# Kernel optimization log

Hardware: AMD Instinct MI355X
Metric: run time of the kernel (lower is better)

## Reference

```python
import jax, jax.numpy as jnp
import numpy as np

N = 50000      # nodes
E = 600000     # edges
D = 128        # feature dim (ninput == noutput -> residual)
GN = 5000      # graph_node_size (10 graphs)
GE = 60000     # graph_edge_size
EPS_NORM = 1e-5
EPS_RED = 1e-6


def graph_norm(x, size, gamma, beta):
    # torch.split into equal graphs, per-graph mean / (std(ddof=1) + eps)
    G = x.shape[0] // size
    xr = x.reshape(G, size, -1)
    mean = xr.mean(axis=1, keepdims=True)
    std = jnp.std(xr, axis=1, keepdims=True, ddof=1)  # torch.std is unbiased
    out = ((xr - mean) / (std + EPS_NORM)).reshape(x.shape)
    return gamma * out + beta


def setup_inputs() -> dict:
    key = jax.random.key(0)
    ks = jax.random.split(key, 10)
    h = jax.random.normal(ks[0], (N, D), dtype=jnp.float32)
    e = jax.random.normal(ks[1], (E, D), dtype=jnp.float32)
    src = jax.random.randint(ks[2], (E,), 0, N, dtype=jnp.int32)
    dst = jax.random.randint(ks[3], (E,), 0, N, dtype=jnp.int32)
    snorm_n = jnp.ones((1,), jnp.float32)
    snorm_e = jnp.ones((1,), jnp.float32)
    # 5 Linear layers (fc1..fc5), stored as [in, out] so y = x @ W + b
    W = jax.random.normal(ks[4], (5, D, D), dtype=jnp.float32) * (1.0 / np.sqrt(D))
    b = jax.random.normal(ks[5], (5, D), dtype=jnp.float32) * 0.01
    gamma_h = jnp.ones((D,), jnp.float32)
    beta_h = jnp.zeros((D,), jnp.float32)
    gamma_e = jnp.ones((D,), jnp.float32)
    beta_e = jnp.zeros((D,), jnp.float32)
    return {"h": h, "e": e, "src": src, "dst": dst,
            "snorm_n": snorm_n, "snorm_e": snorm_e,
            "W": W, "b": b,
            "gamma_h": gamma_h, "beta_h": beta_h,
            "gamma_e": gamma_e, "beta_e": beta_e}


def reference(h, e, src, dst, snorm_n, snorm_e, W, b, gamma_h, beta_h, gamma_e, beta_e):
    h_in, e_in = h, e
    Ah = h @ W[0] + b[0]
    Bh = h @ W[1] + b[1]
    Ce = e @ W[2] + b[2]
    Dh = h @ W[3] + b[3]
    Eh = h @ W[4] + b[4]

    # message: e_ij = Ce + Dh[src] + Eh[dst]
    e_new = Ce + Dh[src] + Eh[dst]              # [E, D]
    sig = jax.nn.sigmoid(e_new)
    num = jax.ops.segment_sum(sig * Bh[src], dst, num_segments=N)   # [N, D]
    den = jax.ops.segment_sum(sig, dst, num_segments=N)             # [N, D]
    deg = jax.ops.segment_sum(jnp.ones((E, 1), h.dtype), dst, num_segments=N)
    h_agg = Ah + num / (den + EPS_RED)
    # DGL leaves zero-in-degree nodes untouched (keep original h)
    h_new = jnp.where(deg > 0, h_agg, h)

    h_new = h_new * snorm_n
    h_new = jax.nn.relu(graph_norm(h_new, GN, gamma_h, beta_h))
    e_out = e_new * snorm_e
    e_out = jax.nn.relu(graph_norm(e_out, GE, gamma_e, beta_e))

    # residual (ninput == noutput); dropout is identity in eval mode
    h_new = h_in + h_new
    e_out = e_in + e_out
    return (h_new, e_out)
```

## Files before the change

### kernel.cpp

```cpp
#include <hip/hip_runtime.h>
#include <math.h>

#define NNODES 50000
#define NEDGES 600000
#define DIM 128
#define GNSZ 5000
#define GESZ 60000
#define NDTOT (NNODES*DIM)
#define EPS_NORM 1e-5f
#define EPS_RED  1e-6f

union F4 { float4 v; float f[4]; };

__device__ __forceinline__ float4 ld4(const float* p){ return *(const float4*)p; }

__global__ __launch_bounds__(256) void k1_node_gemm(
    const float* __restrict__ h, const float* __restrict__ W, const float* __restrict__ bias,
    float* __restrict__ Ah, float* __restrict__ Bh, float* __restrict__ Dh, float* __restrict__ Eh)
{
  __shared__ float as[32][129];
  const int t = threadIdx.x;
  const int base = blockIdx.x * 32;
  #pragma unroll
  for (int i = 0; i < 4; i++){
    int f = t + i*256;
    int row = f >> 5, c4 = (f & 31) * 4;
    float4 v = make_float4(0.f,0.f,0.f,0.f);
    if (base + row < NNODES) v = ld4(h + (size_t)(base+row)*DIM + c4);
    as[row][c4+0]=v.x; as[row][c4+1]=v.y; as[row][c4+2]=v.z; as[row][c4+3]=v.w;
  }
  __syncthreads();
  const int tcol = t & 31, trow = t >> 5;
  float* outp[4] = {Ah, Bh, Dh, Eh};
  const int mats[4] = {0,1,3,4};
  #pragma unroll 1
  for (int mi = 0; mi < 4; mi++){
    const float* Wm = W + mats[mi]*(DIM*DIM);
    float acc[4][4];
    #pragma unroll
    for (int i=0;i<4;i++){
      #pragma unroll
      for (int j=0;j<4;j++) acc[i][j]=0.f;
    }
    #pragma unroll 4
    for (int k = 0; k < DIM; k++){
      F4 bv; bv.v = ld4(Wm + k*DIM + tcol*4);
      float a0 = as[trow*4+0][k], a1 = as[trow*4+1][k];
      float a2 = as[trow*4+2][k], a3 = as[trow*4+3][k];
      #pragma unroll
      for (int j=0;j<4;j++){
        acc[0][j] += a0*bv.f[j]; acc[1][j] += a1*bv.f[j];
        acc[2][j] += a2*bv.f[j]; acc[3][j] += a3*bv.f[j];
      }
    }
    F4 bb; bb.v = ld4(bias + mats[mi]*DIM + tcol*4);
    #pragma unroll
    for (int i=0;i<4;i++){
      int row = base + trow*4 + i;
      if (row < NNODES){
        F4 o;
        #pragma unroll
        for (int j=0;j<4;j++) o.f[j] = acc[i][j] + bb.f[j];
        *(float4*)(outp[mi] + (size_t)row*DIM + tcol*4) = o.v;
      }
    }
  }
}

__global__ void k_hist(const int* __restrict__ dst, int* __restrict__ deg)
{
  int i = blockIdx.x*256 + threadIdx.x;
  if (i < NEDGES) atomicAdd(&deg[dst[i]], 1);
}

__global__ void k_scan(const int* __restrict__ deg, int* __restrict__ off)
{
  __shared__ int tot[256];
  const int t = threadIdx.x;
  const int CH = (NNODES + 255) / 256;
  const int base = t * CH;
  int s = 0;
  for (int k = 0; k < CH; k++){
    int i = base + k;
    if (i < NNODES) s += deg[i];
  }
  tot[t] = s;
  __syncthreads();
  for (int d = 1; d < 256; d <<= 1){
    int w = (t >= d) ? tot[t-d] : 0;
    __syncthreads();
    tot[t] += w;
    __syncthreads();
  }
  int run = tot[t] - s;
  for (int k = 0; k < CH; k++){
    int i = base + k;
    if (i < NNODES){ off[i] = run; run += deg[i]; }
  }
  if (t == 255) off[NNODES] = run;
}

__global__ void k_scatter(const int* __restrict__ dst, const int* __restrict__ off,
                          int* __restrict__ cur, int* __restrict__ eidx)
{
  int i = blockIdx.x*256 + threadIdx.x;
  if (i < NEDGES){
    int d = dst[i];
    int p = atomicAdd(&cur[d], 1);
    eidx[off[d] + p] = i;
  }
}

__global__ __launch_bounds__(256) void k2_edge(
    const float* __restrict__ e, const int* __restrict__ src, const int* __restrict__ dst,
    const float* __restrict__ W, const float* __restrict__ bias,
    const float* __restrict__ Dh, const float* __restrict__ Eh,
    const float* __restrict__ snorm_e,
    float* __restrict__ e_new,
    float* __restrict__ sum_e, float* __restrict__ sumsq_e)
{
  __shared__ float as[32][129];
  __shared__ int ssrc[32], sdst[32];
  __shared__ float s_sum[128], s_sq[128];
  const int t = threadIdx.x;
  const int base = blockIdx.x * 32;
  if (t < 128){ s_sum[t]=0.f; s_sq[t]=0.f; }
  if (t >= 128 && t < 160) ssrc[t-128] = src[base + t - 128];
  if (t >= 160 && t < 192) sdst[t-160] = dst[base + t - 160];
  #pragma unroll
  for (int i = 0; i < 4; i++){
    int f = t + i*256;
    int row = f >> 5, c4 = (f & 31)*4;
    float4 v = ld4(e + (size_t)(base+row)*DIM + c4);
    as[row][c4+0]=v.x; as[row][c4+1]=v.y; as[row][c4+2]=v.z; as[row][c4+3]=v.w;
  }
  __syncthreads();
  const int tcol = t & 31, trow = t >> 5;
  const float* W2 = W + 2*(DIM*DIM);
  float acc[4][4];
  #pragma unroll
  for (int i=0;i<4;i++){
    #pragma unroll
    for (int j=0;j<4;j++) acc[i][j]=0.f;
  }
  #pragma unroll 4
  for (int k = 0; k < DIM; k++){
    F4 bv; bv.v = ld4(W2 + k*DIM + tcol*4);
    float a0 = as[trow*4+0][k], a1 = as[trow*4+1][k];
    float a2 = as[trow*4+2][k], a3 = as[trow*4+3][k];
    #pragma unroll
    for (int j=0;j<4;j++){
      acc[0][j] += a0*bv.f[j]; acc[1][j] += a1*bv.f[j];
      acc[2][j] += a2*bv.f[j]; acc[3][j] += a3*bv.f[j];
    }
  }
  F4 b2; b2.v = ld4(bias + 2*DIM + tcol*4);
  const float sn = snorm_e[0];
  float lsum[4] = {0,0,0,0}, lsq[4] = {0,0,0,0};
  #pragma unroll
  for (int i=0;i<4;i++){
    int el = trow*4 + i;
    int sgl = ssrc[el], dgl = sdst[el];
    F4 dh;  dh.v  = ld4(Dh + (size_t)sgl*DIM + tcol*4);
    F4 ehv; ehv.v = ld4(Eh + (size_t)dgl*DIM + tcol*4);
    F4 o;
    #pragma unroll
    for (int j=0;j<4;j++) o.f[j] = acc[i][j] + b2.f[j] + dh.f[j] + ehv.f[j];
    *(float4*)(e_new + (size_t)(base+el)*DIM + tcol*4) = o.v;
    #pragma unroll
    for (int j=0;j<4;j++){
      float x = o.f[j]*sn;
      lsum[j] += x; lsq[j] += x*x;
    }
  }
  #pragma unroll
  for (int j=0;j<4;j++){
    atomicAdd(&s_sum[tcol*4+j], lsum[j]);
    atomicAdd(&s_sq[tcol*4+j],  lsq[j]);
  }
  __syncthreads();
  if (t < 128){
    int g = base / GESZ;
    atomicAdd(&sum_e[g*DIM + t],  s_sum[t]);
    atomicAdd(&sumsq_e[g*DIM + t], s_sq[t]);
  }
}

__global__ __launch_bounds__(256) void k_agg(
    const float* __restrict__ h,
    const float* __restrict__ e_new,
    const float* __restrict__ Bh,
    const int* __restrict__ src,
    const int* __restrict__ off,
    const int* __restrict__ eidx,
    const float* __restrict__ snorm_n,
    float* hbuf,
    float* __restrict__ sum_h, float* __restrict__ sumsq_h)
{
  __shared__ float s_sum[128], s_sq[128];
  const int t = threadIdx.x;
  if (t < 128){ s_sum[t]=0.f; s_sq[t]=0.f; }
  __syncthreads();
  int idx4 = blockIdx.x*256 + t;
  int node = idx4 >> 5;
  int c4 = (idx4 & 31) * 4;
  size_t offp = (size_t)node*DIM + c4;
  const int beg = off[node], end = off[node+1];
  float num[4] = {0,0,0,0}, den[4] = {0,0,0,0};
  int eid = (beg < end) ? eidx[beg] : 0;
  for (int k = beg; k < end; k++){
    int eidn = (k+1 < end) ? eidx[k+1] : 0;
    int s = src[eid];
    F4 ev; ev.v = ld4(e_new + (size_t)eid*DIM + c4);
    F4 bh; bh.v = ld4(Bh + (size_t)s*DIM + c4);
    #pragma unroll
    for (int j=0;j<4;j++){
      float sig = 1.f/(1.f + __expf(-ev.f[j]));
      num[j] += sig * bh.f[j];
      den[j] += sig;
    }
    eid = eidn;
  }
  F4 a;  a.v  = *(float4*)(hbuf + offp);
  F4 hh; hh.v = ld4(h + offp);
  const float sn = snorm_n[0];
  const bool hasdeg = (end > beg);
  F4 x;
  #pragma unroll
  for (int j=0;j<4;j++){
    float v = hasdeg ? (a.f[j] + num[j]/(den[j] + EPS_RED)) : hh.f[j];
    x.f[j] = v * sn;
  }
  *(float4*)(hbuf + offp) = x.v;
  #pragma unroll
  for (int j=0;j<4;j++){
    atomicAdd(&s_sum[c4+j], x.f[j]);
    atomicAdd(&s_sq[c4+j],  x.f[j]*x.f[j]);
  }
  __syncthreads();
  if (t < 128){
    int g = (blockIdx.x*8) / GNSZ;
    atomicAdd(&sum_h[g*DIM+t],   s_sum[t]);
    atomicAdd(&sumsq_h[g*DIM+t], s_sq[t]);
  }
}

__global__ void k4_finalize(float* __restrict__ stats)
{
  int idx = blockIdx.x*256 + threadIdx.x;
  if (idx >= 2560) return;
  int which = idx / 1280;
  int i = idx - which*1280;
  float n = which ? (float)GNSZ : (float)GESZ;
  float s  = stats[which*2560 + i];
  float sq = stats[which*2560 + 1280 + i];
  float mean = s / n;
  float var = (sq - s*s/n) / (n - 1.f);
  var = fmaxf(var, 0.f);
  float inv = 1.f / (sqrtf(var) + EPS_NORM);
  stats[5120 + which*2560 + i] = mean;
  stats[5120 + which*2560 + 1280 + i] = inv;
}

__global__ __launch_bounds__(256) void k5_norm_h(
    const float* __restrict__ h_in, const float* __restrict__ gamma, const float* __restrict__ beta,
    const float* __restrict__ stats, float* outp)
{
  int idx4 = blockIdx.x*256 + threadIdx.x;
  int node = idx4 >> 5;
  int c4 = (idx4 & 31)*4;
  int g = node / GNSZ;
  size_t off = (size_t)node*DIM + c4;
  F4 x;  x.v  = *(float4*)(outp + off);
  F4 mn; mn.v = ld4(stats + 7680 + g*DIM + c4);
  F4 iv; iv.v = ld4(stats + 8960 + g*DIM + c4);
  F4 gm; gm.v = ld4(gamma + c4);
  F4 bt; bt.v = ld4(beta + c4);
  F4 hi; hi.v = ld4(h_in + off);
  F4 o;
  #pragma unroll
  for (int j=0;j<4;j++){
    float y = gm.f[j]*((x.f[j]-mn.f[j])*iv.f[j]) + bt.f[j];
    o.f[j] = hi.f[j] + fmaxf(y, 0.f);
  }
  *(float4*)(outp + off) = o.v;
}

__global__ __launch_bounds__(256) void k5_norm_e(
    const float* __restrict__ e_in, const float* __restrict__ gamma, const float* __restrict__ beta,
    const float* __restrict__ snorm_e, const float* __restrict__ stats, float* outp)
{
  int idx4 = blockIdx.x*256 + threadIdx.x;
  int edge = idx4 >> 5;
  int c4 = (idx4 & 31)*4;
  int g = edge / GESZ;
  size_t off = (size_t)edge*DIM + c4;
  const float sn = snorm_e[0];
  F4 x;  x.v  = *(float4*)(outp + off);
  F4 mn; mn.v = ld4(stats + 5120 + g*DIM + c4);
  F4 iv; iv.v = ld4(stats + 6400 + g*DIM + c4);
  F4 gm; gm.v = ld4(gamma + c4);
  F4 bt; bt.v = ld4(beta + c4);
  F4 ei; ei.v = ld4(e_in + off);
  F4 o;
  #pragma unroll
  for (int j=0;j<4;j++){
    float xx = x.f[j]*sn;
    float y = gm.f[j]*((xx-mn.f[j])*iv.f[j]) + bt.f[j];
    o.f[j] = ei.f[j] + fmaxf(y, 0.f);
  }
  *(float4*)(outp + off) = o.v;
}

extern "C" void kernel_launch(void* const* d_in, const int* in_sizes, int n_in,
                              void* d_out, int out_size, void* d_ws, size_t ws_size,
                              hipStream_t stream)
{
  (void)in_sizes; (void)n_in; (void)out_size; (void)ws_size;
  const float* h    = (const float*)d_in[0];
  const float* e    = (const float*)d_in[1];
  const int*   src  = (const int*)d_in[2];
  const int*   dst  = (const int*)d_in[3];
  const float* snorm_n = (const float*)d_in[4];
  const float* snorm_e = (const float*)d_in[5];
  const float* W    = (const float*)d_in[6];
  const float* bias = (const float*)d_in[7];
  const float* gamma_h = (const float*)d_in[8];
  const float* beta_h  = (const float*)d_in[9];
  const float* gamma_e = (const float*)d_in[10];
  const float* beta_e  = (const float*)d_in[11];

  float* out_h = (float*)d_out;
  float* out_e = out_h + (size_t)NDTOT;
  float* ws  = (float*)d_ws;
  float* Bh  = ws;
  float* Dh  = ws + 1*(size_t)NDTOT;
  float* Eh  = ws + 2*(size_t)NDTOT;
  float* stats = ws + 3*(size_t)NDTOT;
  int* ints  = (int*)(stats + 10240);
  int* ideg  = ints;
  int* icur  = ints + NNODES;
  int* ioff  = ints + 2*NNODES;
  int* ieidx = ints + 3*NNODES + 1;

  hipMemsetAsync(stats, 0, 5120*sizeof(float), stream);
  hipMemsetAsync(ints, 0, 2*(size_t)NNODES*sizeof(int), stream);

  k_hist<<<(NEDGES+255)/256, 256, 0, stream>>>(dst, ideg);
  k_scan<<<1, 256, 0, stream>>>(ideg, ioff);
  k_scatter<<<(NEDGES+255)/256, 256, 0, stream>>>(dst, ioff, icur, ieidx);

  k1_node_gemm<<<1563, 256, 0, stream>>>(h, W, bias, out_h, Bh, Dh, Eh);
  k2_edge<<<18750, 256, 0, stream>>>(e, src, dst, W, bias, Dh, Eh, snorm_e,
                                     out_e, stats, stats+1280);
  k_agg<<<6250, 256, 0, stream>>>(h, out_e, Bh, src, ioff, ieidx, snorm_n,
                                  out_h, stats+2560, stats+3840);
  k4_finalize<<<10, 256, 0, stream>>>(stats);
  k5_norm_h<<<6250, 256, 0, stream>>>(h, gamma_h, beta_h, stats, out_h);
  k5_norm_e<<<75000, 256, 0, stream>>>(e, gamma_e, beta_e, snorm_e, stats, out_e);
}
```

Before: 1.550 ms.

## Use split-bf16 MFMA for node and edge linear layers

Replaces the scalar FP32 GEMMs in the node and edge kernels with MFMA 16x16x32 bf16 instructions. Each FP32 value is split into bf16 hi and lo parts and combined with three MFMAs to keep accuracy close to FP32. Weights are pre-packed into the MFMA fragment layout by a new small kernel, and block sizes change to 96 rows with 384 threads. Output stores become scalar column-strided writes instead of float4, which may reduce store coalescing.

Result: faster. 1.411 ms (-9.0%).

```diff
diff --git a/kernel.cpp b/kernel.cpp
--- a/kernel.cpp
+++ b/kernel.cpp
@@ -14,54 +14,108 @@
 
 __device__ __forceinline__ float4 ld4(const float* p){ return *(const float4*)p; }
 
-__global__ __launch_bounds__(256) void k1_node_gemm(
-    const float* __restrict__ h, const float* __restrict__ W, const float* __restrict__ bias,
+typedef __attribute__((ext_vector_type(8))) short short8;
+typedef __attribute__((ext_vector_type(4))) float f32x4;
+
+union U8 { short8 v; unsigned short u[8]; };
+
+__device__ __forceinline__ unsigned short f2bf(float x){
+  unsigned u = __float_as_uint(x);
+  u += 0x7FFFu + ((u >> 16) & 1u);
+  return (unsigned short)(u >> 16);
+}
+__device__ __forceinline__ float bf2f(unsigned short b){
+  return __uint_as_float(((unsigned)b) << 16);
+}
+
+__global__ __launch_bounds__(256) void k0_pack(
+    const float* __restrict__ W,
+    unsigned short* __restrict__ Whi, unsigned short* __restrict__ Wlo)
+{
+  int slot = blockIdx.x*256 + threadIdx.x;
+  if (slot >= 10240) return;
+  int lane = slot & 63;
+  int ct   = (slot >> 6) & 7;
+  int ks   = (slot >> 9) & 3;
+  int mat  = slot >> 11;
+  int g = lane >> 4;
+  int col = ct*16 + (lane & 15);
+  U8 ho, lo;
+  #pragma unroll
+  for (int e = 0; e < 8; e++){
+    int k = ks*32 + g*8 + e;
+    float x = W[mat*DIM*DIM + k*DIM + col];
+    unsigned short hb = f2bf(x);
+    ho.u[e] = hb;
+    lo.u[e] = f2bf(x - bf2f(hb));
+  }
+  *(short8*)(Whi + (size_t)slot*8) = ho.v;
+  *(short8*)(Wlo + (size_t)slot*8) = lo.v;
+}
+
+__global__ __launch_bounds__(384) void k1_node_gemm(
+    const float* __restrict__ h,
+    const unsigned short* __restrict__ Whi, const unsigned short* __restrict__ Wlo,
+    const float* __restrict__ bias,
     float* __restrict__ Ah, float* __restrict__ Bh, float* __restrict__ Dh, float* __restrict__ Eh)
 {
-  __shared__ float as[32][129];
   const int t = threadIdx.x;
-  const int base = blockIdx.x * 32;
-  #pragma unroll
-  for (int i = 0; i < 4; i++){
-    int f = t + i*256;
-    int row = f >> 5, c4 = (f & 31) * 4;
-    float4 v = make_float4(0.f,0.f,0.f,0.f);
-    if (base + row < NNODES) v = ld4(h + (size_t)(base+row)*DIM + c4);
-    as[row][c4+0]=v.x; as[row][c4+1]=v.y; as[row][c4+2]=v.z; as[row][c4+3]=v.w;
-  }
-  __syncthreads();
-  const int tcol = t & 31, trow = t >> 5;
+  const int w = t >> 6, l = t & 63;
+  const int g = l >> 4, lr = l & 15;
+  const int rbase = blockIdx.x*96 + w*16;
+  const int rowA = rbase + lr;
+
+  short8 ahi[4], alo[4];
+  #pragma unroll
+  for (int ks = 0; ks < 4; ks++){
+    F4 q0, q1;
+    if (rowA < NNODES){
+      q0.v = ld4(h + (size_t)rowA*DIM + ks*32 + g*8);
+      q1.v = ld4(h + (size_t)rowA*DIM + ks*32 + g*8 + 4);
+    } else {
+      q0.v = make_float4(0.f,0.f,0.f,0.f); q1.v = q0.v;
+    }
+    U8 ah, al;
+    #pragma unroll
+    for (int j = 0; j < 4; j++){
+      unsigned short hb = f2bf(q0.f[j]);
+      ah.u[j] = hb; al.u[j] = f2bf(q0.f[j] - bf2f(hb));
+      hb = f2bf(q1.f[j]);
+      ah.u[4+j] = hb; al.u[4+j] = f2bf(q1.f[j] - bf2f(hb));
+    }
+    ahi[ks] = ah.v; alo[ks] = al.v;
+  }
+
+  const int mats[4] = {0,1,3,4};
   float* outp[4] = {Ah, Bh, Dh, Eh};
-  const int mats[4] = {0,1,3,4};
   #pragma unroll 1
   for (int mi = 0; mi < 4; mi++){
-    const float* Wm = W + mats[mi]*(DIM*DIM);
-    float acc[4][4];
-    #pragma unroll
-    for (int i=0;i<4;i++){
+    f32x4 acc[8];
+    #pragma unroll
+    for (int ct = 0; ct < 8; ct++) acc[ct] = (f32x4){0.f,0.f,0.f,0.f};
+    #pragma unroll
+    for (int ks = 0; ks < 4; ks++){
+      const size_t fbase = (size_t)(mats[mi]*4 + ks)*4096 + (size_t)l*8;
       #pragma unroll
-      for (int j=0;j<4;j++) acc[i][j]=0.f;
-    }
-    #pragma unroll 4
-    for (int k = 0; k < DIM; k++){
-      F4 bv; bv.v = ld4(Wm + k*DIM + tcol*4);
-      float a0 = as[trow*4+0][k], a1 = as[trow*4+1][k];
-      float a2 = as[trow*4+2][k], a3 = as[trow*4+3][k];
-      #pragma unroll
-      for (int j=0;j<4;j++){
-        acc[0][j] += a0*bv.f[j]; acc[1][j] += a1*bv.f[j];
-        acc[2][j] += a2*bv.f[j]; acc[3][j] += a3*bv.f[j];
+      for (int ct = 0; ct < 8; ct++){
+        short8 bhi = *(const short8*)(Whi + fbase + ct*512);
+        short8 blo = *(const short8*)(Wlo + fbase + ct*512);
+        acc[ct] = __builtin_amdgcn_mfma_f32_16x16x32_bf16(ahi[ks], bhi, acc[ct], 0,0,0);
+        acc[ct] = __builtin_amdgcn_mfma_f32_16x16x32_bf16(alo[ks], bhi, acc[ct], 0,0,0);
+        acc[ct] = __builtin_amdgcn_mfma_f32_16x16x32_bf16(ahi[ks], blo, acc[ct], 0,0,0);
       }
     }
-    F4 bb; bb.v = ld4(bias + mats[mi]*DIM + tcol*4);
-    #pragma unroll
-    for (int i=0;i<4;i++){
-      int row = base + trow*4 + i;
+    const float* bb = bias + mats[mi]*DIM;
+    #pragma unroll
+    for (int r = 0; r < 4; r++){
+      int row = rbase + g*4 + r;
       if (row < NNODES){
-        F4 o;
+        float* op = outp[mi] + (size_t)row*DIM;
         #pragma unroll
-        for (int j=0;j<4;j++) o.f[j] = acc[i][j] + bb.f[j];
-        *(float4*)(outp[mi] + (size_t)row*DIM + tcol*4) = o.v;
+        for (int ct = 0; ct < 8; ct++){
+          int col = ct*16 + lr;
+          op[col] = acc[ct][r] + bb[col];
+        }
       }
     }
   }
@@ -87,9 +141,9 @@
   tot[t] = s;
   __syncthreads();
   for (int d = 1; d < 256; d <<= 1){
-    int w = (t >= d) ? tot[t-d] : 0;
+    int wv = (t >= d) ? tot[t-d] : 0;
     __syncthreads();
-    tot[t] += w;
+    tot[t] += wv;
     __syncthreads();
   }
   int run = tot[t] - s;
@@ -111,78 +165,88 @@
   }
 }
 
-__global__ __launch_bounds__(256) void k2_edge(
+__global__ __launch_bounds__(384) void k2_edge(
     const float* __restrict__ e, const int* __restrict__ src, const int* __restrict__ dst,
-    const float* __restrict__ W, const float* __restrict__ bias,
+    const unsigned short* __restrict__ Whi, const unsigned short* __restrict__ Wlo,
+    const float* __restrict__ bias,
     const float* __restrict__ Dh, const float* __restrict__ Eh,
     const float* __restrict__ snorm_e,
     float* __restrict__ e_new,
     float* __restrict__ sum_e, float* __restrict__ sumsq_e)
 {
-  __shared__ float as[32][129];
-  __shared__ int ssrc[32], sdst[32];
+  __shared__ int ssrc[96], sdst[96];
   __shared__ float s_sum[128], s_sq[128];
   const int t = threadIdx.x;
-  const int base = blockIdx.x * 32;
-  if (t < 128){ s_sum[t]=0.f; s_sq[t]=0.f; }
-  if (t >= 128 && t < 160) ssrc[t-128] = src[base + t - 128];
-  if (t >= 160 && t < 192) sdst[t-160] = dst[base + t - 160];
-  #pragma unroll
-  for (int i = 0; i < 4; i++){
-    int f = t + i*256;
-    int row = f >> 5, c4 = (f & 31)*4;
-    float4 v = ld4(e + (size_t)(base+row)*DIM + c4);
-    as[row][c4+0]=v.x; as[row][c4+1]=v.y; as[row][c4+2]=v.z; as[row][c4+3]=v.w;
-  }
+  const int base = blockIdx.x * 96;
+  if (t < 96) ssrc[t] = src[base + t];
+  else if (t < 192) sdst[t-96] = dst[base + t - 96];
+  else if (t < 320){ s_sum[t-192] = 0.f; s_sq[t-192] = 0.f; }
   __syncthreads();
-  const int tcol = t & 31, trow = t >> 5;
-  const float* W2 = W + 2*(DIM*DIM);
-  float acc[4][4];
-  #pragma unroll
-  for (int i=0;i<4;i++){
-    #pragma unroll
-    for (int j=0;j<4;j++) acc[i][j]=0.f;
-  }
-  #pragma unroll 4
-  for (int k = 0; k < DIM; k++){
-    F4 bv; bv.v = ld4(W2 + k*DIM + tcol*4);
-    float a0 = as[trow*4+0][k], a1 = as[trow*4+1][k];
-    float a2 = as[trow*4+2][k], a3 = as[trow*4+3][k];
-    #pragma unroll
-    for (int j=0;j<4;j++){
-      acc[0][j] += a0*bv.f[j]; acc[1][j] += a1*bv.f[j];
-      acc[2][j] += a2*bv.f[j]; acc[3][j] += a3*bv.f[j];
-    }
-  }
-  F4 b2; b2.v = ld4(bias + 2*DIM + tcol*4);
+
+  const int w = t >> 6, l = t & 63, g = l >> 4, lr = l & 15;
+  const int rowA = base + w*16 + lr;
+
+  f32x4 acc[8];
+  #pragma unroll
+  for (int ct = 0; ct < 8; ct++) acc[ct] = (f32x4){0.f,0.f,0.f,0.f};
+
+  #pragma unroll
+  for (int ks = 0; ks < 4; ks++){
+    F4 q0, q1;
+    q0.v = ld4(e + (size_t)rowA*DIM + ks*32 + g*8);
+    q1.v = ld4(e + (size_t)rowA*DIM + ks*32 + g*8 + 4);
+    U8 ah, al;
+    #pragma unroll
+    for (int j = 0; j < 4; j++){
+      unsigned short hb = f2bf(q0.f[j]);
+      ah.u[j] = hb; al.u[j] = f2bf(q0.f[j] - bf2f(hb));
+      hb = f2bf(q1.f[j]);
+      ah.u[4+j] = hb; al.u[4+j] = f2bf(q1.f[j] - bf2f(hb));
+    }
+    const size_t fbase = (size_t)(2*4 + ks)*4096 + (size_t)l*8;
+    #pragma unroll
+    for (int ct = 0; ct < 8; ct++){
+      short8 bhi = *(const short8*)(Whi + fbase + ct*512);
+      short8 blo = *(const short8*)(Wlo + fbase + ct*512);
+      acc[ct] = __builtin_amdgcn_mfma_f32_16x16x32_bf16(ah.v, bhi, acc[ct], 0,0,0);
+      acc[ct] = __builtin_amdgcn_mfma_f32_16x16x32_bf16(al.v, bhi, acc[ct], 0,0,0);
+      acc[ct] = __builtin_amdgcn_mfma_f32_16x16x32_bf16(ah.v, blo, acc[ct], 0,0,0);
+    }
+  }
+
   const float sn = snorm_e[0];
-  float lsum[4] = {0,0,0,0}, lsq[4] = {0,0,0,0};
-  #pragma unroll
-  for (int i=0;i<4;i++){
-    int el = trow*4 + i;
-    int sgl = ssrc[el], dgl = sdst[el];
-    F4 dh;  dh.v  = ld4(Dh + (size_t)sgl*DIM + tcol*4);
-    F4 ehv; ehv.v = ld4(Eh + (size_t)dgl*DIM + tcol*4);
-    F4 o;
-    #pragma unroll
-    for (int j=0;j<4;j++) o.f[j] = acc[i][j] + b2.f[j] + dh.f[j] + ehv.f[j];
-    *(float4*)(e_new + (size_t)(base+el)*DIM + tcol*4) = o.v;
-    #pragma unroll
-    for (int j=0;j<4;j++){
-      float x = o.f[j]*sn;
-      lsum[j] += x; lsq[j] += x*x;
-    }
-  }
-  #pragma unroll
-  for (int j=0;j<4;j++){
-    atomicAdd(&s_sum[tcol*4+j], lsum[j]);
-    atomicAdd(&s_sq[tcol*4+j],  lsq[j]);
+  const float* b2 = bias + 2*DIM;
+  float lsum[8], lsq[8];
+  #pragma unroll
+  for (int ct = 0; ct < 8; ct++){ lsum[ct] = 0.f; lsq[ct] = 0.f; }
+
+  #pragma unroll
+  for (int r = 0; r < 4; r++){
+    int erow = w*16 + g*4 + r;
+    int edge = base + erow;
+    int sgl = ssrc[erow], dgl = sdst[erow];
+    const float* dp = Dh + (size_t)sgl*DIM;
+    const float* ep = Eh + (size_t)dgl*DIM;
+    float* op = e_new + (size_t)edge*DIM;
+    #pragma unroll
+    for (int ct = 0; ct < 8; ct++){
+      int col = ct*16 + lr;
+      float v = acc[ct][r] + b2[col] + dp[col] + ep[col];
+      op[col] = v;
+      float x = v*sn;
+      lsum[ct] += x; lsq[ct] += x*x;
+    }
+  }
+  #pragma unroll
+  for (int ct = 0; ct < 8; ct++){
+    atomicAdd(&s_sum[ct*16 + lr], lsum[ct]);
+    atomicAdd(&s_sq[ct*16 + lr],  lsq[ct]);
   }
   __syncthreads();
   if (t < 128){
-    int g = base / GESZ;
-    atomicAdd(&sum_e[g*DIM + t],  s_sum[t]);
-    atomicAdd(&sumsq_e[g*DIM + t], s_sq[t]);
+    int gg = base / GESZ;
+    atomicAdd(&sum_e[gg*DIM + t],   s_sum[t]);
+    atomicAdd(&sumsq_e[gg*DIM + t], s_sq[t]);
   }
 }
 
@@ -337,7 +401,9 @@
   float* Dh  = ws + 1*(size_t)NDTOT;
   float* Eh  = ws + 2*(size_t)NDTOT;
   float* stats = ws + 3*(size_t)NDTOT;
-  int* ints  = (int*)(stats + 10240);
+  unsigned short* Whi = (unsigned short*)(stats + 10240);
+  unsigned short* Wlo = Whi + 81920;
+  int* ints  = (int*)(Wlo + 81920);
   int* ideg  = ints;
   int* icur  = ints + NNODES;
   int* ioff  = ints + 2*NNODES;
@@ -346,13 +412,14 @@
   hipMemsetAsync(stats, 0, 5120*sizeof(float), stream);
   hipMemsetAsync(ints, 0, 2*(size_t)NNODES*sizeof(int), stream);
 
+  k0_pack<<<40, 256, 0, stream>>>(W, Whi, Wlo);
   k_hist<<<(NEDGES+255)/256, 256, 0, stream>>>(dst, ideg);
   k_scan<<<1, 256, 0, stream>>>(ideg, ioff);
   k_scatter<<<(NEDGES+255)/256, 256, 0, stream>>>(dst, ioff, icur, ieidx);
 
-  k1_node_gemm<<<1563, 256, 0, stream>>>(h, W, bias, out_h, Bh, Dh, Eh);
-  k2_edge<<<18750, 256, 0, stream>>>(e, src, dst, W, bias, Dh, Eh, snorm_e,
-                                     out_e, stats, stats+1280);
+  k1_node_gemm<<<521, 384, 0, stream>>>(h, Whi, Wlo, bias, out_h, Bh, Dh, Eh);
+  k2_edge<<<6250, 384, 0, stream>>>(e, src, dst, Whi, Wlo, bias, Dh, Eh, snorm_e,
+                                    out_e, stats, stats+1280);
   k_agg<<<6250, 256, 0, stream>>>(h, out_e, Bh, src, ioff, ieidx, snorm_n,
                                   out_h, stats+2560, stats+3840);
   k4_finalize<<<10, 256, 0, stream>>>(stats);
```
